# Kernel tuning notes

Hardware: AMD Instinct MI355X
Metric: run time of the kernel (lower is better)

The kernel has to match this reference:

```python
import jax, jax.numpy as jnp
import numpy as np


def setup_inputs() -> dict:
    key = jax.random.key(0)
    k1, k2, k3, k4 = jax.random.split(key, 4)
    n, b, h, f = 8, 64, 128, 256
    hs = 64
    x = jax.random.normal(k1, (n, b, h, f), dtype=jnp.float32)
    # torch Linear weights are (out, in); store transposed as (in, out) for x @ W
    Wq = jax.random.normal(k2, (f, hs), dtype=jnp.float32) * (6.0 / (f + hs)) ** 0.5
    Wk = jax.random.normal(k3, (f, hs), dtype=jnp.float32) * (6.0 / (f + hs)) ** 0.5
    Wv = jax.random.normal(k4, (f, hs), dtype=jnp.float32) * (6.0 / (f + hs)) ** 0.5
    return {"x": x, "Wq": Wq, "Wk": Wk, "Wv": Wv}


def reference(x, Wq, Wk, Wv):
    # x: (n, b, h, f). NOTE: scale uses f = n_embd (as in the source), not head_size.
    f = x.shape[-1]
    scale = f ** (-0.5)
    Q = jnp.einsum('nbhf,fd->nbhd', x, Wq)  # (n, b, h, hs)
    K = jnp.einsum('nbhf,fd->nbhd', x, Wk)
    V = jnp.einsum('nbhf,fd->nbhd', x, Wv)
    # alphas[i, j, b, p, q] = sum_d Q[j,b,p,d] * K[i,b,q,d] * scale
    scores = jnp.einsum('jbpd,ibqd->ijbpq', Q, K) * scale  # (n, n, b, h, h)
    alphas = jax.nn.softmax(scores, axis=-1)
    # out[i, j, b, p, d] = sum_q alphas[i,j,b,p,q] V[i,b,q,d]; then sum over i
    o = jnp.einsum('ijbpq,ibqd->jbpd', alphas, V)  # (n, b, h, hs)
    return o
```

## Files before the change

kernel.cpp:

```cpp
#include <hip/hip_runtime.h>
#include <cstdint>

#define N_SEQ 8
#define B_DIM 64
#define H_DIM 128
#define F_DIM 256
#define HS 64

typedef __attribute__((ext_vector_type(8))) short short8;
typedef __attribute__((ext_vector_type(4))) float floatx4;

__device__ __forceinline__ ushort f2bf(float f) {
    union { float f; uint32_t u; } v; v.f = f;
    uint32_t r = v.u + 0x7FFF + ((v.u >> 16) & 1);
    return (ushort)(r >> 16);
}

__device__ __forceinline__ void async_ld16(const ushort* g, ushort* lds) {
    __builtin_amdgcn_global_load_lds(
        (const __attribute__((address_space(1))) unsigned int*)g,
        (__attribute__((address_space(3))) unsigned int*)lds,
        16, 0, 0);
}

__global__ __launch_bounds__(256) void prep_w(
    const float* __restrict__ Wq, const float* __restrict__ Wk,
    const float* __restrict__ Wv, ushort* __restrict__ Wtb)
{
    const int n = blockIdx.x;
    const float* W = (n < 64) ? Wq : (n < 128) ? Wk : Wv;
    const int c = n & 63;
    const int k = threadIdx.x;
    Wtb[n * 256 + k] = f2bf(W[k * 64 + c]);
}

#define XS_STRIDE 264
__global__ __launch_bounds__(256, 4) void proj_mfma(
    const float* __restrict__ x, const ushort* __restrict__ Wtb,
    ushort* __restrict__ Qb, ushort* __restrict__ Kb, ushort* __restrict__ Vtb)
{
    __shared__ ushort xs[64 * XS_STRIDE];
    const int t = threadIdx.x;
    const int blk = blockIdx.x;
    const int64_t row0 = (int64_t)blk * 64;

    const float4* xg = (const float4*)(x + row0 * F_DIM);
    #pragma unroll
    for (int u = 0; u < 8; ++u) {
        const int idx = t + 256 * u;
        const int row = idx >> 5;
        const int c8 = (idx & 31) * 8;
        const float4 a = xg[idx * 2];
        const float4 b = xg[idx * 2 + 1];
        *(ushort4*)&xs[row * XS_STRIDE + c8] =
            make_ushort4(f2bf(a.x), f2bf(a.y), f2bf(a.z), f2bf(a.w));
        *(ushort4*)&xs[row * XS_STRIDE + c8 + 4] =
            make_ushort4(f2bf(b.x), f2bf(b.y), f2bf(b.z), f2bf(b.w));
    }
    __syncthreads();

    const int w = t >> 6, lane = t & 63;
    const int q16 = lane >> 4, l16 = lane & 15;
    const int n0 = w * 48;

    floatx4 acc[4][3];
    #pragma unroll
    for (int mt = 0; mt < 4; ++mt)
        #pragma unroll
        for (int nt = 0; nt < 3; ++nt) acc[mt][nt] = (floatx4){0.f, 0.f, 0.f, 0.f};

    short8 nb[3];
    #pragma unroll
    for (int nt = 0; nt < 3; ++nt)
        nb[nt] = *(const short8*)&Wtb[(n0 + nt * 16 + l16) * 256 + q16 * 8];

    for (int ks = 0; ks < 8; ++ks) {
        short8 cur[3];
        #pragma unroll
        for (int nt = 0; nt < 3; ++nt) cur[nt] = nb[nt];
        if (ks < 7) {
            #pragma unroll
            for (int nt = 0; nt < 3; ++nt)
                nb[nt] = *(const short8*)&Wtb[(n0 + nt * 16 + l16) * 256 + (ks + 1) * 32 + q16 * 8];
        }
        #pragma unroll
        for (int mt = 0; mt < 4; ++mt) {
            const short8 afr = *(const short8*)&xs[(mt * 16 + l16) * XS_STRIDE + ks * 32 + q16 * 8];
            #pragma unroll
            for (int nt = 0; nt < 3; ++nt)
                acc[mt][nt] = __builtin_amdgcn_mfma_f32_16x16x32_bf16(afr, cur[nt], acc[mt][nt], 0, 0, 0);
        }
    }

    const float qscale = 0.0625f * 1.44269504f;
    #pragma unroll
    for (int mt = 0; mt < 4; ++mt) {
        const int64_t g = row0 + mt * 16 + q16 * 4;
        #pragma unroll
        for (int nt = 0; nt < 3; ++nt) {
            const int ntb = n0 + nt * 16;
            const int n = ntb + l16;
            if (ntb < 64) {
                #pragma unroll
                for (int r = 0; r < 4; ++r)
                    Qb[(g + r) * 64 + n] = f2bf(acc[mt][nt][r] * qscale);
            } else if (ntb < 128) {
                #pragma unroll
                for (int r = 0; r < 4; ++r)
                    Kb[(g + r) * 64 + (n - 64)] = f2bf(acc[mt][nt][r]);
            } else {
                const int d = n - 128;
                const int ib = (int)(g >> 7);
                const int h = (int)(g & 127);
                *(ushort4*)&Vtb[((int64_t)(ib * 64 + d)) * 128 + h] =
                    make_ushort4(f2bf(acc[mt][nt][0]), f2bf(acc[mt][nt][1]),
                                 f2bf(acc[mt][nt][2]), f2bf(acc[mt][nt][3]));
            }
        }
    }
}

#define PT_STRIDE 40
__global__ __launch_bounds__(256, 2) void attn_mfma(
    const ushort* __restrict__ Qb, const ushort* __restrict__ Kb,
    const ushort* __restrict__ Vtb, float* __restrict__ out)
{
    __shared__ ushort Ks[2][8192];
    __shared__ ushort Vt[2][8192];
    __shared__ ushort Ps[4][2][16 * PT_STRIDE];

    const int t = threadIdx.x;
    const int blk = blockIdx.x;
    const int b  = ((blk & 7) << 3) | ((blk >> 3) & 7);
    const int j  = blk >> 6;
    const int jb = j * 64 + b;

    const int w = t >> 6, lane = t & 63;
    const int q16 = lane >> 4, l16 = lane & 15;

    int koff[4], voff[4], ldsoff[4];
    #pragma unroll
    for (int u = 0; u < 4; ++u) {
        const int fi = w * 4 + u;
        koff[u] = ((fi & 7) * 16 + l16) * 64 + (fi >> 3) * 32 + q16 * 8;
        voff[u] = ((fi & 3) * 16 + l16) * 128 + (fi >> 2) * 32 + q16 * 8;
        ldsoff[u] = fi * 512;
    }

    const int prow = jb * H_DIM + w * 16 + l16;
    short8 qa[2][2];
    #pragma unroll
    for (int hh = 0; hh < 2; ++hh)
        #pragma unroll
        for (int ks = 0; ks < 2; ++ks)
            qa[hh][ks] = *(const short8*)&Qb[(prow + hh * 64) * 64 + ks * 32 + q16 * 8];

    floatx4 of[2][4];
    #pragma unroll
    for (int hh = 0; hh < 2; ++hh)
        #pragma unroll
        for (int mt = 0; mt < 4; ++mt) of[hh][mt] = (floatx4){0.f, 0.f, 0.f, 0.f};

    {
        const ushort* kg = Kb + ((0 * B_DIM + b) << 13);
        const ushort* vg = Vtb + ((0 * B_DIM + b) << 13);
        #pragma unroll
        for (int u = 0; u < 4; ++u) {
            const int lo = __builtin_amdgcn_readfirstlane(ldsoff[u]);
            async_ld16(kg + koff[u], &Ks[0][lo]);
            async_ld16(vg + voff[u], &Vt[0][lo]);
        }
    }

    for (int i = 0; i < N_SEQ; ++i) {
        const int buf = i & 1;
        __syncthreads();

        if (i < N_SEQ - 1) {
            const ushort* kg = Kb + (((i + 1) * B_DIM + b) << 13);
            const ushort* vg = Vtb + (((i + 1) * B_DIM + b) << 13);
            #pragma unroll
            for (int u = 0; u < 4; ++u) {
                const int lo = __builtin_amdgcn_readfirstlane(ldsoff[u]);
                async_ld16(kg + koff[u], &Ks[buf ^ 1][lo]);
                async_ld16(vg + voff[u], &Vt[buf ^ 1][lo]);
            }
        }

        floatx4 sf[2][8];
        #pragma unroll
        for (int hh = 0; hh < 2; ++hh)
            #pragma unroll
            for (int nt = 0; nt < 8; ++nt) sf[hh][nt] = (floatx4){0.f, 0.f, 0.f, 0.f};
        #pragma unroll
        for (int ks = 0; ks < 2; ++ks)
            #pragma unroll
            for (int nt = 0; nt < 8; ++nt) {
                const short8 ak = *(const short8*)&Ks[buf][(ks * 8 + nt) * 512 + lane * 8];
                sf[0][nt] = __builtin_amdgcn_mfma_f32_16x16x32_bf16(ak, qa[0][ks], sf[0][nt], 0, 0, 0);
                sf[1][nt] = __builtin_amdgcn_mfma_f32_16x16x32_bf16(ak, qa[1][ks], sf[1][nt], 0, 0, 0);
            }

        float inv[2];
        #pragma unroll
        for (int hh = 0; hh < 2; ++hh) {
            float l = 0.f;
            #pragma unroll
            for (int nt = 0; nt < 8; ++nt)
                #pragma unroll
                for (int r = 0; r < 4; ++r) {
                    sf[hh][nt][r] = __builtin_amdgcn_exp2f(sf[hh][nt][r]);
                    l += sf[hh][nt][r];
                }
            l += __shfl_xor(l, 16);
            l += __shfl_xor(l, 32);
            inv[hh] = __builtin_amdgcn_rcpf(l);
        }

        #pragma unroll
        for (int kq = 0; kq < 4; ++kq) {
            #pragma unroll
            for (int hh = 0; hh < 2; ++hh)
                #pragma unroll
                for (int tt = 0; tt < 2; ++tt) {
                    const int nt = kq * 2 + tt;
                    *(ushort4*)&Ps[w][hh][l16 * PT_STRIDE + tt * 16 + q16 * 4] =
                        make_ushort4(f2bf(sf[hh][nt][0] * inv[hh]),
                                     f2bf(sf[hh][nt][1] * inv[hh]),
                                     f2bf(sf[hh][nt][2] * inv[hh]),
                                     f2bf(sf[hh][nt][3] * inv[hh]));
                }
            const short8 bp0 = *(const short8*)&Ps[w][0][l16 * PT_STRIDE + q16 * 8];
            const short8 bp1 = *(const short8*)&Ps[w][1][l16 * PT_STRIDE + q16 * 8];
            #pragma unroll
            for (int mt = 0; mt < 4; ++mt) {
                const short8 av = *(const short8*)&Vt[buf][(kq * 4 + mt) * 512 + lane * 8];
                of[0][mt] = __builtin_amdgcn_mfma_f32_16x16x32_bf16(av, bp0, of[0][mt], 0, 0, 0);
                of[1][mt] = __builtin_amdgcn_mfma_f32_16x16x32_bf16(av, bp1, of[1][mt], 0, 0, 0);
            }
        }
    }

    #pragma unroll
    for (int hh = 0; hh < 2; ++hh)
        #pragma unroll
        for (int mt = 0; mt < 4; ++mt)
            *(float4*)&out[(int64_t)(prow + hh * 64) * HS + mt * 16 + q16 * 4] =
                make_float4(of[hh][mt][0], of[hh][mt][1], of[hh][mt][2], of[hh][mt][3]);
}

extern "C" void kernel_launch(void* const* d_in, const int* in_sizes, int n_in,
                              void* d_out, int out_size, void* d_ws, size_t ws_size,
                              hipStream_t stream)
{
    const float* x  = (const float*)d_in[0];
    const float* Wq = (const float*)d_in[1];
    const float* Wk = (const float*)d_in[2];
    const float* Wv = (const float*)d_in[3];
    float* out = (float*)d_out;

    const size_t qkv = (size_t)N_SEQ * B_DIM * H_DIM * HS;
    ushort* Qb  = (ushort*)d_ws;
    ushort* Kb  = Qb + qkv;
    ushort* Vtb = Kb + qkv;
    ushort* Wtb = Vtb + qkv;

    prep_w<<<192, 256, 0, stream>>>(Wq, Wk, Wv, Wtb);
    proj_mfma<<<(N_SEQ * B_DIM * H_DIM) / 64, 256, 0, stream>>>(x, Wtb, Qb, Kb, Vtb);
    attn_mfma<<<N_SEQ * B_DIM, 256, 0, stream>>>(Qb, Kb, Vtb, out);
}
```

Before: 148.7 us.

## Stream projection from global without LDS and defer softmax normalization in attention

The projection kernel drops the LDS staging of x. Each wave now loads its own 16 rows straight from global, converts them to bf16 in registers, and computes the 192 outputs in two passes of six tiles with double-buffered weight fragments. The attention kernel interleaves QK^T, exp and PV per 32-column chunk into a separate accumulator and applies the reciprocal row sum once at the end of each i step. This cuts live score registers and removes the barrier for x, but it reloads x from global twice per wave and adds an extra accumulate step.

After: 180.0 us. 1.21x slower.

```diff
diff --git a/kernel.cpp b/kernel.cpp
--- a/kernel.cpp
+++ b/kernel.cpp
@@ -34,87 +34,75 @@
     Wtb[n * 256 + k] = f2bf(W[k * 64 + c]);
 }
 
-#define XS_STRIDE 264
 __global__ __launch_bounds__(256, 4) void proj_mfma(
     const float* __restrict__ x, const ushort* __restrict__ Wtb,
     ushort* __restrict__ Qb, ushort* __restrict__ Kb, ushort* __restrict__ Vtb)
 {
-    __shared__ ushort xs[64 * XS_STRIDE];
     const int t = threadIdx.x;
-    const int blk = blockIdx.x;
-    const int64_t row0 = (int64_t)blk * 64;
-
-    const float4* xg = (const float4*)(x + row0 * F_DIM);
-    #pragma unroll
-    for (int u = 0; u < 8; ++u) {
-        const int idx = t + 256 * u;
-        const int row = idx >> 5;
-        const int c8 = (idx & 31) * 8;
-        const float4 a = xg[idx * 2];
-        const float4 b = xg[idx * 2 + 1];
-        *(ushort4*)&xs[row * XS_STRIDE + c8] =
-            make_ushort4(f2bf(a.x), f2bf(a.y), f2bf(a.z), f2bf(a.w));
-        *(ushort4*)&xs[row * XS_STRIDE + c8 + 4] =
-            make_ushort4(f2bf(b.x), f2bf(b.y), f2bf(b.z), f2bf(b.w));
-    }
-    __syncthreads();
-
     const int w = t >> 6, lane = t & 63;
     const int q16 = lane >> 4, l16 = lane & 15;
-    const int n0 = w * 48;
-
-    floatx4 acc[4][3];
-    #pragma unroll
-    for (int mt = 0; mt < 4; ++mt)
-        #pragma unroll
-        for (int nt = 0; nt < 3; ++nt) acc[mt][nt] = (floatx4){0.f, 0.f, 0.f, 0.f};
-
-    short8 nb[3];
-    #pragma unroll
-    for (int nt = 0; nt < 3; ++nt)
-        nb[nt] = *(const short8*)&Wtb[(n0 + nt * 16 + l16) * 256 + q16 * 8];
-
-    for (int ks = 0; ks < 8; ++ks) {
-        short8 cur[3];
-        #pragma unroll
-        for (int nt = 0; nt < 3; ++nt) cur[nt] = nb[nt];
-        if (ks < 7) {
-            #pragma unroll
-            for (int nt = 0; nt < 3; ++nt)
-                nb[nt] = *(const short8*)&Wtb[(n0 + nt * 16 + l16) * 256 + (ks + 1) * 32 + q16 * 8];
-        }
-        #pragma unroll
-        for (int mt = 0; mt < 4; ++mt) {
-            const short8 afr = *(const short8*)&xs[(mt * 16 + l16) * XS_STRIDE + ks * 32 + q16 * 8];
-            #pragma unroll
-            for (int nt = 0; nt < 3; ++nt)
-                acc[mt][nt] = __builtin_amdgcn_mfma_f32_16x16x32_bf16(afr, cur[nt], acc[mt][nt], 0, 0, 0);
-        }
-    }
-
+    const int64_t row0w = (int64_t)blockIdx.x * 64 + w * 16;
+
+    const float* __restrict__ xrow = x + (row0w + l16) * F_DIM;
     const float qscale = 0.0625f * 1.44269504f;
-    #pragma unroll
-    for (int mt = 0; mt < 4; ++mt) {
-        const int64_t g = row0 + mt * 16 + q16 * 4;
-        #pragma unroll
-        for (int nt = 0; nt < 3; ++nt) {
-            const int ntb = n0 + nt * 16;
-            const int n = ntb + l16;
-            if (ntb < 64) {
+
+    #pragma unroll 1
+    for (int pass = 0; pass < 2; ++pass) {
+        const int nbase = pass * 96;
+
+        floatx4 acc[6];
+        #pragma unroll
+        for (int nt = 0; nt < 6; ++nt) acc[nt] = (floatx4){0.f, 0.f, 0.f, 0.f};
+
+        short8 b0[6], b1[6];
+        #pragma unroll
+        for (int nt = 0; nt < 6; ++nt)
+            b0[nt] = *(const short8*)&Wtb[(nbase + nt * 16 + l16) * 256 + q16 * 8];
+        float4 a0 = *(const float4*)&xrow[q16 * 8];
+        float4 a1 = *(const float4*)&xrow[q16 * 8 + 4];
+
+        #pragma unroll
+        for (int ks = 0; ks < 8; ++ks) {
+            const float4 ca0 = a0, ca1 = a1;
+            short8* cur = (ks & 1) ? b1 : b0;
+            short8* nxt = (ks & 1) ? b0 : b1;
+            if (ks < 7) {
+                a0 = *(const float4*)&xrow[(ks + 1) * 32 + q16 * 8];
+                a1 = *(const float4*)&xrow[(ks + 1) * 32 + q16 * 8 + 4];
+                #pragma unroll
+                for (int nt = 0; nt < 6; ++nt)
+                    nxt[nt] = *(const short8*)&Wtb[(nbase + nt * 16 + l16) * 256 + (ks + 1) * 32 + q16 * 8];
+            }
+            union { short8 s; ushort u[8]; } af;
+            af.u[0] = f2bf(ca0.x); af.u[1] = f2bf(ca0.y);
+            af.u[2] = f2bf(ca0.z); af.u[3] = f2bf(ca0.w);
+            af.u[4] = f2bf(ca1.x); af.u[5] = f2bf(ca1.y);
+            af.u[6] = f2bf(ca1.z); af.u[7] = f2bf(ca1.w);
+            #pragma unroll
+            for (int nt = 0; nt < 6; ++nt)
+                acc[nt] = __builtin_amdgcn_mfma_f32_16x16x32_bf16(af.s, cur[nt], acc[nt], 0, 0, 0);
+        }
+
+        const int64_t g = row0w + q16 * 4;
+        #pragma unroll
+        for (int nt = 0; nt < 6; ++nt) {
+            const int nb = nbase + nt * 16;
+            const int n = nb + l16;
+            if (nb < 64) {
                 #pragma unroll
                 for (int r = 0; r < 4; ++r)
-                    Qb[(g + r) * 64 + n] = f2bf(acc[mt][nt][r] * qscale);
-            } else if (ntb < 128) {
+                    Qb[(g + r) * 64 + n] = f2bf(acc[nt][r] * qscale);
+            } else if (nb < 128) {
                 #pragma unroll
                 for (int r = 0; r < 4; ++r)
-                    Kb[(g + r) * 64 + (n - 64)] = f2bf(acc[mt][nt][r]);
+                    Kb[(g + r) * 64 + (n - 64)] = f2bf(acc[nt][r]);
             } else {
                 const int d = n - 128;
                 const int ib = (int)(g >> 7);
                 const int h = (int)(g & 127);
                 *(ushort4*)&Vtb[((int64_t)(ib * 64 + d)) * 128 + h] =
-                    make_ushort4(f2bf(acc[mt][nt][0]), f2bf(acc[mt][nt][1]),
-                                 f2bf(acc[mt][nt][2]), f2bf(acc[mt][nt][3]));
+                    make_ushort4(f2bf(acc[nt][0]), f2bf(acc[nt][1]),
+                                 f2bf(acc[nt][2]), f2bf(acc[nt][3]));
             }
         }
     }
@@ -162,8 +150,8 @@
         for (int mt = 0; mt < 4; ++mt) of[hh][mt] = (floatx4){0.f, 0.f, 0.f, 0.f};
 
     {
-        const ushort* kg = Kb + ((0 * B_DIM + b) << 13);
-        const ushort* vg = Vtb + ((0 * B_DIM + b) << 13);
+        const ushort* kg = Kb + ((int64_t)b << 13);
+        const ushort* vg = Vtb + ((int64_t)b << 13);
         #pragma unroll
         for (int u = 0; u < 4; ++u) {
             const int lo = __builtin_amdgcn_readfirstlane(ldsoff[u]);
@@ -177,8 +165,8 @@
         __syncthreads();
 
         if (i < N_SEQ - 1) {
-            const ushort* kg = Kb + (((i + 1) * B_DIM + b) << 13);
-            const ushort* vg = Vtb + (((i + 1) * B_DIM + b) << 13);
+            const ushort* kg = Kb + ((int64_t)((i + 1) * B_DIM + b) << 13);
+            const ushort* vg = Vtb + ((int64_t)((i + 1) * B_DIM + b) << 13);
             #pragma unroll
             for (int u = 0; u < 4; ++u) {
                 const int lo = __builtin_amdgcn_readfirstlane(ldsoff[u]);
@@ -187,57 +175,63 @@
             }
         }
 
-        floatx4 sf[2][8];
+        float l[2] = {0.f, 0.f};
+        floatx4 pv[2][4];
         #pragma unroll
         for (int hh = 0; hh < 2; ++hh)
             #pragma unroll
-            for (int nt = 0; nt < 8; ++nt) sf[hh][nt] = (floatx4){0.f, 0.f, 0.f, 0.f};
-        #pragma unroll
-        for (int ks = 0; ks < 2; ++ks)
-            #pragma unroll
-            for (int nt = 0; nt < 8; ++nt) {
-                const short8 ak = *(const short8*)&Ks[buf][(ks * 8 + nt) * 512 + lane * 8];
-                sf[0][nt] = __builtin_amdgcn_mfma_f32_16x16x32_bf16(ak, qa[0][ks], sf[0][nt], 0, 0, 0);
-                sf[1][nt] = __builtin_amdgcn_mfma_f32_16x16x32_bf16(ak, qa[1][ks], sf[1][nt], 0, 0, 0);
-            }
-
-        float inv[2];
-        #pragma unroll
-        for (int hh = 0; hh < 2; ++hh) {
-            float l = 0.f;
-            #pragma unroll
-            for (int nt = 0; nt < 8; ++nt)
-                #pragma unroll
-                for (int r = 0; r < 4; ++r) {
-                    sf[hh][nt][r] = __builtin_amdgcn_exp2f(sf[hh][nt][r]);
-                    l += sf[hh][nt][r];
+            for (int mt = 0; mt < 4; ++mt) pv[hh][mt] = (floatx4){0.f, 0.f, 0.f, 0.f};
+
+        #pragma unroll
+        for (int kq = 0; kq < 4; ++kq) {
+            floatx4 sc[2][2];
+            #pragma unroll
+            for (int hh = 0; hh < 2; ++hh)
+                #pragma unroll
+                for (int tt = 0; tt < 2; ++tt) sc[hh][tt] = (floatx4){0.f, 0.f, 0.f, 0.f};
+            #pragma unroll
+            for (int ks = 0; ks < 2; ++ks)
+                #pragma unroll
+                for (int tt = 0; tt < 2; ++tt) {
+                    const short8 ak = *(const short8*)&Ks[buf][(ks * 8 + kq * 2 + tt) * 512 + lane * 8];
+                    sc[0][tt] = __builtin_amdgcn_mfma_f32_16x16x32_bf16(ak, qa[0][ks], sc[0][tt], 0, 0, 0);
+                    sc[1][tt] = __builtin_amdgcn_mfma_f32_16x16x32_bf16(ak, qa[1][ks], sc[1][tt], 0, 0, 0);
                 }
-            l += __shfl_xor(l, 16);
-            l += __shfl_xor(l, 32);
-            inv[hh] = __builtin_amdgcn_rcpf(l);
-        }
-
-        #pragma unroll
-        for (int kq = 0; kq < 4; ++kq) {
+
             #pragma unroll
             for (int hh = 0; hh < 2; ++hh)
                 #pragma unroll
                 for (int tt = 0; tt < 2; ++tt) {
-                    const int nt = kq * 2 + tt;
+                    const float e0 = __builtin_amdgcn_exp2f(sc[hh][tt][0]);
+                    const float e1 = __builtin_amdgcn_exp2f(sc[hh][tt][1]);
+                    const float e2 = __builtin_amdgcn_exp2f(sc[hh][tt][2]);
+                    const float e3 = __builtin_amdgcn_exp2f(sc[hh][tt][3]);
+                    l[hh] += (e0 + e1) + (e2 + e3);
                     *(ushort4*)&Ps[w][hh][l16 * PT_STRIDE + tt * 16 + q16 * 4] =
-                        make_ushort4(f2bf(sf[hh][nt][0] * inv[hh]),
-                                     f2bf(sf[hh][nt][1] * inv[hh]),
-                                     f2bf(sf[hh][nt][2] * inv[hh]),
-                                     f2bf(sf[hh][nt][3] * inv[hh]));
+                        make_ushort4(f2bf(e0), f2bf(e1), f2bf(e2), f2bf(e3));
                 }
+
             const short8 bp0 = *(const short8*)&Ps[w][0][l16 * PT_STRIDE + q16 * 8];
             const short8 bp1 = *(const short8*)&Ps[w][1][l16 * PT_STRIDE + q16 * 8];
             #pragma unroll
             for (int mt = 0; mt < 4; ++mt) {
                 const short8 av = *(const short8*)&Vt[buf][(kq * 4 + mt) * 512 + lane * 8];
-                of[0][mt] = __builtin_amdgcn_mfma_f32_16x16x32_bf16(av, bp0, of[0][mt], 0, 0, 0);
-                of[1][mt] = __builtin_amdgcn_mfma_f32_16x16x32_bf16(av, bp1, of[1][mt], 0, 0, 0);
-            }
+                pv[0][mt] = __builtin_amdgcn_mfma_f32_16x16x32_bf16(av, bp0, pv[0][mt], 0, 0, 0);
+                pv[1][mt] = __builtin_amdgcn_mfma_f32_16x16x32_bf16(av, bp1, pv[1][mt], 0, 0, 0);
+            }
+        }
+
+        #pragma unroll
+        for (int hh = 0; hh < 2; ++hh) {
+            float lt = l[hh];
+            lt += __shfl_xor(lt, 16);
+            lt += __shfl_xor(lt, 32);
+            const float inv = __builtin_amdgcn_rcpf(lt);
+            #pragma unroll
+            for (int mt = 0; mt < 4; ++mt)
+                #pragma unroll
+                for (int r = 0; r < 4; ++r)
+                    of[hh][mt][r] = fmaf(inv, pv[hh][mt][r], of[hh][mt][r]);
         }
     }
 
```

## Stream QK^T per key chunk with deferred softmax normalization and deeper weight prefetch

Applied to the files above, without the earlier changes.

The attention loop now computes scores one 32-key chunk at a time, exponentiates them, writes unnormalized P to LDS and accumulates P·V into a per-block accumulator. The row-sum reciprocal is applied once at the end through an FMA into the output. This cuts the register footprint of holding all 8 score tiles and lets QK, exp and PV overlap. It also changes rounding, because P is stored as bf16 before normalization. The projection kernel now prefetches weight fragments three k-steps ahead instead of one, with the k-loop fully unrolled, and K/V address offsets are computed in 64-bit.

Result: no change. 149.5 us (+0.5%).

```diff
diff --git a/kernel.cpp b/kernel.cpp
--- a/kernel.cpp
+++ b/kernel.cpp
@@ -69,19 +69,22 @@
         #pragma unroll
         for (int nt = 0; nt < 3; ++nt) acc[mt][nt] = (floatx4){0.f, 0.f, 0.f, 0.f};
 
-    short8 nb[3];
-    #pragma unroll
-    for (int nt = 0; nt < 3; ++nt)
-        nb[nt] = *(const short8*)&Wtb[(n0 + nt * 16 + l16) * 256 + q16 * 8];
-
+    short8 bq[3][3];
+    #pragma unroll
+    for (int s = 0; s < 3; ++s)
+        #pragma unroll
+        for (int nt = 0; nt < 3; ++nt)
+            bq[s][nt] = *(const short8*)&Wtb[(n0 + nt * 16 + l16) * 256 + s * 32 + q16 * 8];
+
+    #pragma unroll
     for (int ks = 0; ks < 8; ++ks) {
         short8 cur[3];
         #pragma unroll
-        for (int nt = 0; nt < 3; ++nt) cur[nt] = nb[nt];
-        if (ks < 7) {
+        for (int nt = 0; nt < 3; ++nt) cur[nt] = bq[ks % 3][nt];
+        if (ks < 5) {
             #pragma unroll
             for (int nt = 0; nt < 3; ++nt)
-                nb[nt] = *(const short8*)&Wtb[(n0 + nt * 16 + l16) * 256 + (ks + 1) * 32 + q16 * 8];
+                bq[ks % 3][nt] = *(const short8*)&Wtb[(n0 + nt * 16 + l16) * 256 + (ks + 3) * 32 + q16 * 8];
         }
         #pragma unroll
         for (int mt = 0; mt < 4; ++mt) {
@@ -162,8 +165,8 @@
         for (int mt = 0; mt < 4; ++mt) of[hh][mt] = (floatx4){0.f, 0.f, 0.f, 0.f};
 
     {
-        const ushort* kg = Kb + ((0 * B_DIM + b) << 13);
-        const ushort* vg = Vtb + ((0 * B_DIM + b) << 13);
+        const ushort* kg = Kb + ((int64_t)b << 13);
+        const ushort* vg = Vtb + ((int64_t)b << 13);
         #pragma unroll
         for (int u = 0; u < 4; ++u) {
             const int lo = __builtin_amdgcn_readfirstlane(ldsoff[u]);
@@ -177,8 +180,8 @@
         __syncthreads();
 
         if (i < N_SEQ - 1) {
-            const ushort* kg = Kb + (((i + 1) * B_DIM + b) << 13);
-            const ushort* vg = Vtb + (((i + 1) * B_DIM + b) << 13);
+            const ushort* kg = Kb + ((int64_t)((i + 1) * B_DIM + b) << 13);
+            const ushort* vg = Vtb + ((int64_t)((i + 1) * B_DIM + b) << 13);
             #pragma unroll
             for (int u = 0; u < 4; ++u) {
                 const int lo = __builtin_amdgcn_readfirstlane(ldsoff[u]);
@@ -187,57 +190,63 @@
             }
         }
 
-        floatx4 sf[2][8];
+        float l[2] = {0.f, 0.f};
+        floatx4 pv[2][4];
         #pragma unroll
         for (int hh = 0; hh < 2; ++hh)
             #pragma unroll
-            for (int nt = 0; nt < 8; ++nt) sf[hh][nt] = (floatx4){0.f, 0.f, 0.f, 0.f};
-        #pragma unroll
-        for (int ks = 0; ks < 2; ++ks)
-            #pragma unroll
-            for (int nt = 0; nt < 8; ++nt) {
-                const short8 ak = *(const short8*)&Ks[buf][(ks * 8 + nt) * 512 + lane * 8];
-                sf[0][nt] = __builtin_amdgcn_mfma_f32_16x16x32_bf16(ak, qa[0][ks], sf[0][nt], 0, 0, 0);
-                sf[1][nt] = __builtin_amdgcn_mfma_f32_16x16x32_bf16(ak, qa[1][ks], sf[1][nt], 0, 0, 0);
-            }
-
-        float inv[2];
-        #pragma unroll
-        for (int hh = 0; hh < 2; ++hh) {
-            float l = 0.f;
-            #pragma unroll
-            for (int nt = 0; nt < 8; ++nt)
-                #pragma unroll
-                for (int r = 0; r < 4; ++r) {
-                    sf[hh][nt][r] = __builtin_amdgcn_exp2f(sf[hh][nt][r]);
-                    l += sf[hh][nt][r];
+            for (int mt = 0; mt < 4; ++mt) pv[hh][mt] = (floatx4){0.f, 0.f, 0.f, 0.f};
+
+        #pragma unroll
+        for (int kq = 0; kq < 4; ++kq) {
+            floatx4 sc[2][2];
+            #pragma unroll
+            for (int hh = 0; hh < 2; ++hh)
+                #pragma unroll
+                for (int tt = 0; tt < 2; ++tt) sc[hh][tt] = (floatx4){0.f, 0.f, 0.f, 0.f};
+            #pragma unroll
+            for (int ks = 0; ks < 2; ++ks)
+                #pragma unroll
+                for (int tt = 0; tt < 2; ++tt) {
+                    const short8 ak = *(const short8*)&Ks[buf][(ks * 8 + kq * 2 + tt) * 512 + lane * 8];
+                    sc[0][tt] = __builtin_amdgcn_mfma_f32_16x16x32_bf16(ak, qa[0][ks], sc[0][tt], 0, 0, 0);
+                    sc[1][tt] = __builtin_amdgcn_mfma_f32_16x16x32_bf16(ak, qa[1][ks], sc[1][tt], 0, 0, 0);
                 }
-            l += __shfl_xor(l, 16);
-            l += __shfl_xor(l, 32);
-            inv[hh] = __builtin_amdgcn_rcpf(l);
-        }
-
-        #pragma unroll
-        for (int kq = 0; kq < 4; ++kq) {
+
             #pragma unroll
             for (int hh = 0; hh < 2; ++hh)
                 #pragma unroll
                 for (int tt = 0; tt < 2; ++tt) {
-                    const int nt = kq * 2 + tt;
+                    const float e0 = __builtin_amdgcn_exp2f(sc[hh][tt][0]);
+                    const float e1 = __builtin_amdgcn_exp2f(sc[hh][tt][1]);
+                    const float e2 = __builtin_amdgcn_exp2f(sc[hh][tt][2]);
+                    const float e3 = __builtin_amdgcn_exp2f(sc[hh][tt][3]);
+                    l[hh] += (e0 + e1) + (e2 + e3);
                     *(ushort4*)&Ps[w][hh][l16 * PT_STRIDE + tt * 16 + q16 * 4] =
-                        make_ushort4(f2bf(sf[hh][nt][0] * inv[hh]),
-                                     f2bf(sf[hh][nt][1] * inv[hh]),
-                                     f2bf(sf[hh][nt][2] * inv[hh]),
-                                     f2bf(sf[hh][nt][3] * inv[hh]));
+                        make_ushort4(f2bf(e0), f2bf(e1), f2bf(e2), f2bf(e3));
                 }
+
             const short8 bp0 = *(const short8*)&Ps[w][0][l16 * PT_STRIDE + q16 * 8];
             const short8 bp1 = *(const short8*)&Ps[w][1][l16 * PT_STRIDE + q16 * 8];
             #pragma unroll
             for (int mt = 0; mt < 4; ++mt) {
                 const short8 av = *(const short8*)&Vt[buf][(kq * 4 + mt) * 512 + lane * 8];
-                of[0][mt] = __builtin_amdgcn_mfma_f32_16x16x32_bf16(av, bp0, of[0][mt], 0, 0, 0);
-                of[1][mt] = __builtin_amdgcn_mfma_f32_16x16x32_bf16(av, bp1, of[1][mt], 0, 0, 0);
+                pv[0][mt] = __builtin_amdgcn_mfma_f32_16x16x32_bf16(av, bp0, pv[0][mt], 0, 0, 0);
+                pv[1][mt] = __builtin_amdgcn_mfma_f32_16x16x32_bf16(av, bp1, pv[1][mt], 0, 0, 0);
             }
+        }
+
+        #pragma unroll
+        for (int hh = 0; hh < 2; ++hh) {
+            float lt = l[hh];
+            lt += __shfl_xor(lt, 16);
+            lt += __shfl_xor(lt, 32);
+            const float inv = __builtin_amdgcn_rcpf(lt);
+            #pragma unroll
+            for (int mt = 0; mt < 4; ++mt)
+                #pragma unroll
+                for (int r = 0; r < 4; ++r)
+                    of[hh][mt][r] = fmaf(inv, pv[hh][mt][r], of[hh][mt][r]);
         }
     }
 
```
